# Kernel tuning notes

Measured on AMD Instinct MI355X. Metric: run time of the kernel, lower is better.

Reference implementation:

```python
import jax, jax.numpy as jnp
import numpy as np


def setup_inputs() -> dict:
    key = jax.random.key(0)
    ks = jax.random.split(key, 5)
    B, D, U = 16384, 512, 512
    return {
        "inputs": jax.random.normal(ks[0], (B, D), dtype=jnp.float32),
        "h_prev": jax.random.normal(ks[1], (B, U), dtype=jnp.float32),
        "update_kernel": jax.random.normal(ks[2], (D + U, U), dtype=jnp.float32) * 0.03,
        "reset_kernel": jax.random.normal(ks[3], (D + U, U), dtype=jnp.float32) * 0.03,
        "hidden_kernel": jax.random.normal(ks[4], (D + U, U), dtype=jnp.float32) * 0.03,
        "update_bias": jnp.zeros((U,), dtype=jnp.float32),
        "reset_bias": jnp.zeros((U,), dtype=jnp.float32),
        "hidden_bias": jnp.zeros((U,), dtype=jnp.float32),
    }


def reference(inputs, h_prev, update_kernel, reset_kernel, hidden_kernel,
              update_bias, reset_bias, hidden_bias):
    # fused_input: [B, D+U]
    fused = jnp.concatenate([inputs, h_prev], axis=-1)
    zg = jax.nn.sigmoid(fused @ update_kernel + update_bias)   # update gate [B,U]
    rg = jax.nn.sigmoid(fused @ reset_kernel + reset_bias)     # reset gate  [B,U]
    h_tilde = jnp.tanh(
        jnp.concatenate([inputs, rg * h_prev], axis=-1) @ hidden_kernel + hidden_bias
    )
    ht = (1.0 - zg) * h_prev + zg * h_tilde
    return ht
```

## Files before the change

### kernel.cpp

```cpp
#include <hip/hip_runtime.h>
#include <hip/hip_bf16.h>
#include <math.h>

typedef __attribute__((ext_vector_type(4))) float f32x4;
typedef __bf16 bf16x8 __attribute__((ext_vector_type(8)));
typedef unsigned short u16;
typedef void __attribute__((address_space(1))) * as1p;
typedef void __attribute__((address_space(3))) * as3p;

__device__ __forceinline__ unsigned short f2bf(float f) {
    union { float f; unsigned int u; } v; v.f = f;
    unsigned int u = v.u;
    u += 0x7fffu + ((u >> 16) & 1u);
    return (unsigned short)(u >> 16);
}

__device__ __forceinline__ float bf2f(unsigned short b) {
    union { unsigned int u; float f; } v;
    v.u = ((unsigned int)b) << 16;
    return v.f;
}

__device__ __forceinline__ float fast_tanh(float v) {
    float vc = fminf(fmaxf(v, -15.f), 15.f);
    float e = __expf(2.f * vc);
    return (e - 1.f) / (e + 1.f);
}

__global__ void cvt_xh(const float* __restrict__ x, const float* __restrict__ h,
                       u16* __restrict__ xb, u16* __restrict__ hb, int n4) {
    int i = blockIdx.x * blockDim.x + threadIdx.x;
    int stride = gridDim.x * blockDim.x;
    const float4* x4 = (const float4*)x;
    const float4* h4 = (const float4*)h;
    ushort4* xb4 = (ushort4*)xb;
    ushort4* hb4 = (ushort4*)hb;
    for (; i < n4; i += stride) {
        float4 v = x4[i];
        xb4[i] = make_ushort4(f2bf(v.x), f2bf(v.y), f2bf(v.z), f2bf(v.w));
        float4 w = h4[i];
        hb4[i] = make_ushort4(f2bf(w.x), f2bf(w.y), f2bf(w.z), f2bf(w.w));
    }
}

__global__ void tr_cvt3(const float* __restrict__ s0, const float* __restrict__ s1,
                        const float* __restrict__ s2, u16* __restrict__ d0,
                        u16* __restrict__ d1, u16* __restrict__ d2) {
    __shared__ float t[32][33];
    const float* src = (blockIdx.z == 0) ? s0 : (blockIdx.z == 1) ? s1 : s2;
    u16* dst = (blockIdx.z == 0) ? d0 : (blockIdx.z == 1) ? d1 : d2;
    int n0 = blockIdx.x * 32;
    int k0 = blockIdx.y * 32;
    int tx = threadIdx.x, ty = threadIdx.y;
#pragma unroll
    for (int i = 0; i < 4; ++i)
        t[ty + i * 8][tx] = src[(size_t)(k0 + ty + i * 8) * 512 + n0 + tx];
    __syncthreads();
#pragma unroll
    for (int i = 0; i < 4; ++i)
        dst[(size_t)(n0 + ty + i * 8) * 1024 + k0 + tx] = f2bf(t[tx][ty + i * 8]);
}

__device__ __forceinline__ void stage_sw(const u16* g, int gstride, u16* lds, int tid) {
#pragma unroll
    for (int i = 0; i < 4; ++i) {
        int ob = i * 4096 + ((tid >> 6) << 10);
        int o = ob + ((tid & 63) << 4);
        int row = o >> 7;
        int cb = (o & 127) ^ ((row & 7) << 4);
        const u16* gp = g + (size_t)row * gstride + (cb >> 1);
        __builtin_amdgcn_global_load_lds((as1p)(void*)gp, (as3p)(void*)(lds + (ob >> 1)), 16, 0, 0);
    }
}

__device__ __forceinline__ bf16x8 ld_frag(const u16* region, int r, int kb) {
    int byte = (r << 7) + (kb ^ ((r & 7) << 4));
    return *(const bf16x8*)((const char*)region + byte);
}

__device__ __forceinline__ void compute_tile(const u16* LA, const u16* LB,
                                             int wr, int wc, int l, f32x4 (&acc)[4][4]) {
    int fr = l & 15;
    int kbb = (l >> 4) << 4;
#pragma unroll
    for (int q = 0; q < 2; ++q) {
        bf16x8 a[4], b[4];
#pragma unroll
        for (int m = 0; m < 4; ++m)
            a[m] = ld_frag(LA, wr * 64 + m * 16 + fr, q * 64 + kbb);
#pragma unroll
        for (int n = 0; n < 4; ++n)
            b[n] = ld_frag(LB, wc * 64 + n * 16 + fr, q * 64 + kbb);
#pragma unroll
        for (int m = 0; m < 4; ++m)
#pragma unroll
            for (int n = 0; n < 4; ++n)
                acc[m][n] = __builtin_amdgcn_mfma_f32_16x16x32_bf16(a[m], b[n], acc[m][n], 0, 0, 0);
    }
}

template<typename AF, typename BF>
__device__ __forceinline__ void kloop(AF ga, BF gb, u16* lds, int tid,
                                      int wr, int wc, int l, f32x4 (&acc)[4][4]) {
    stage_sw(ga(0), 512, lds, tid);
    stage_sw(gb(0), 1024, lds + 8192, tid);
    __syncthreads();
#pragma unroll
    for (int i = 0; i < 15; ++i) {
        u16* nxt = lds + ((i + 1) & 1) * 16384;
        const u16* cur = lds + (i & 1) * 16384;
        stage_sw(ga(i + 1), 512, nxt, tid);
        stage_sw(gb(i + 1), 1024, nxt + 8192, tid);
        compute_tile(cur, cur + 8192, wr, wc, l, acc);
        __syncthreads();
    }
    compute_tile(lds + 16384, lds + 16384 + 8192, wr, wc, l, acc);
}

__global__ __launch_bounds__(256) void gemm1_k(
    const u16* __restrict__ Xb, const u16* __restrict__ Hb, const u16* __restrict__ Wt,
    const float* __restrict__ ub, const float* __restrict__ rb_,
    u16* __restrict__ zgb, u16* __restrict__ rgh) {
    __shared__ u16 lds[2 * 16384];
    int tid = threadIdx.x;
    int l = tid & 63, w = tid >> 6;
    int wr = w >> 1, wc = w & 1;
    int bidl = blockIdx.x;
    int swz = (bidl & 7) * 128 + (bidl >> 3);
    int mb = swz >> 3, nb = swz & 7;
    int m0 = mb * 128;
    int n0 = nb * 128;
    f32x4 acc[4][4];
#pragma unroll
    for (int m = 0; m < 4; ++m)
#pragma unroll
        for (int n = 0; n < 4; ++n) acc[m][n] = (f32x4){0.f, 0.f, 0.f, 0.f};

    auto ga = [&](int t) -> const u16* {
        return (t < 8) ? (Xb + (size_t)m0 * 512 + t * 64)
                       : (Hb + (size_t)m0 * 512 + (t - 8) * 64);
    };
    auto gb = [&](int t) -> const u16* {
        return Wt + (size_t)n0 * 1024 + t * 64;
    };
    kloop(ga, gb, lds, tid, wr, wc, l, acc);

    int colb = n0 + wc * 64;
    int rowb = m0 + wr * 64 + ((l >> 4) << 2);
    bool isZ = n0 < 512;
#pragma unroll
    for (int n = 0; n < 4; ++n) {
        int col = colb + n * 16 + (l & 15);
        int c = col & 511;
        float bias = isZ ? ub[c] : rb_[c];
#pragma unroll
        for (int m = 0; m < 4; ++m) {
            int row0 = rowb + m * 16;
#pragma unroll
            for (int r = 0; r < 4; ++r) {
                int row = row0 + r;
                float v = acc[m][n][r] + bias;
                float s = 1.f / (1.f + __expf(-v));
                if (isZ) zgb[(size_t)row * 512 + c] = f2bf(s);
                else     rgh[(size_t)row * 512 + c] = f2bf(s * bf2f(Hb[(size_t)row * 512 + c]));
            }
        }
    }
}

__global__ __launch_bounds__(256) void gemm2_k(
    const u16* __restrict__ Xb, const u16* __restrict__ rgh, const u16* __restrict__ Wt,
    const float* __restrict__ hp, const u16* __restrict__ zgb, const float* __restrict__ hb,
    float* __restrict__ out) {
    __shared__ u16 lds[2 * 16384];
    int tid = threadIdx.x;
    int l = tid & 63, w = tid >> 6;
    int wr = w >> 1, wc = w & 1;
    int bidl = blockIdx.x;
    int swz = (bidl & 7) * 64 + (bidl >> 3);
    int mb = swz >> 2, nb = swz & 3;
    int m0 = mb * 128;
    int n0 = nb * 128;
    f32x4 acc[4][4];
#pragma unroll
    for (int m = 0; m < 4; ++m)
#pragma unroll
        for (int n = 0; n < 4; ++n) acc[m][n] = (f32x4){0.f, 0.f, 0.f, 0.f};

    auto ga = [&](int t) -> const u16* {
        return (t < 8) ? (Xb + (size_t)m0 * 512 + t * 64)
                       : (rgh + (size_t)m0 * 512 + (t - 8) * 64);
    };
    auto gb = [&](int t) -> const u16* {
        return Wt + (size_t)n0 * 1024 + t * 64;
    };
    kloop(ga, gb, lds, tid, wr, wc, l, acc);

    int colb = n0 + wc * 64;
    int rowb = m0 + wr * 64 + ((l >> 4) << 2);
#pragma unroll
    for (int n = 0; n < 4; ++n) {
        int col = colb + n * 16 + (l & 15);
        float bias = hb[col];
#pragma unroll
        for (int m = 0; m < 4; ++m) {
            int row0 = rowb + m * 16;
#pragma unroll
            for (int r = 0; r < 4; ++r) {
                int row = row0 + r;
                float v = acc[m][n][r] + bias;
                float t = fast_tanh(v);
                float h0 = hp[(size_t)row * 512 + col];
                float z = bf2f(zgb[(size_t)row * 512 + col]);
                out[(size_t)row * 512 + col] = h0 + z * (t - h0);
            }
        }
    }
}

extern "C" void kernel_launch(void* const* d_in, const int* in_sizes, int n_in,
                              void* d_out, int out_size, void* d_ws, size_t ws_size,
                              hipStream_t stream) {
    const float* x  = (const float*)d_in[0];
    const float* h  = (const float*)d_in[1];
    const float* wz = (const float*)d_in[2];
    const float* wr = (const float*)d_in[3];
    const float* wh = (const float*)d_in[4];
    const float* ub = (const float*)d_in[5];
    const float* rb = (const float*)d_in[6];
    const float* hb = (const float*)d_in[7];
    float* out = (float*)d_out;

    const int B = 16384;
    char* ws = (char*)d_ws;
    size_t off = 0;
    u16* Xb  = (u16*)(ws + off); off += (size_t)B * 512 * 2;
    u16* Hb  = (u16*)(ws + off); off += (size_t)B * 512 * 2;
    u16* Wzr = (u16*)(ws + off); off += (size_t)1024 * 1024 * 2;
    u16* Wht = (u16*)(ws + off); off += (size_t)512 * 1024 * 2;
    u16* rgh = (u16*)(ws + off); off += (size_t)B * 512 * 2;
    u16* zgb = (u16*)(ws + off); off += (size_t)B * 512 * 2;

    cvt_xh<<<2048, 256, 0, stream>>>(x, h, Xb, Hb, B * 512 / 4);

    dim3 tb(32, 8), tg(16, 32, 3);
    tr_cvt3<<<tg, tb, 0, stream>>>(wz, wr, wh, Wzr, Wzr + (size_t)512 * 1024, Wht);

    gemm1_k<<<1024, 256, 0, stream>>>(Xb, Hb, Wzr, ub, rb, zgb, rgh);
    gemm2_k<<<512, 256, 0, stream>>>(Xb, rgh, Wht, h, zgb, hb, out);
}
```

Before: 119.3 us.

## Stage GEMM epilogues through LDS for vectorized stores and split gate kernels

Each GEMM epilogue now writes its accumulators to LDS and rereads them row-major, so bias, activation and global loads and stores run as 8-wide vectors. The aim is to replace the scattered 2- and 4-byte global accesses of the old epilogue with coalesced ones. The fused z/r GEMM is also split into two separate 512-block kernels, which removes the per-element isZ branch. The cost is an extra kernel launch, extra LDS traffic with two barriers, and likely LDS bank conflicts in the scatter step.

```diff
diff --git a/kernel.cpp b/kernel.cpp
--- a/kernel.cpp
+++ b/kernel.cpp
@@ -3,8 +3,10 @@
 #include <math.h>
 
 typedef __attribute__((ext_vector_type(4))) float f32x4;
+typedef __attribute__((ext_vector_type(8))) float f32x8;
 typedef __bf16 bf16x8 __attribute__((ext_vector_type(8)));
 typedef unsigned short u16;
+typedef u16 u16x8 __attribute__((ext_vector_type(8)));
 typedef void __attribute__((address_space(1))) * as1p;
 typedef void __attribute__((address_space(3))) * as3p;
 
@@ -117,19 +119,33 @@
     compute_tile(lds + 16384, lds + 16384 + 8192, wr, wc, l, acc);
 }
 
-__global__ __launch_bounds__(256) void gemm1_k(
+__device__ __forceinline__ void scatter_acc(float* tf, const f32x4 (&acc)[4][4],
+                                            int wr, int wc, int l) {
+    int colb = wc * 64;
+    int rowb = wr * 64 + ((l >> 4) << 2);
+#pragma unroll
+    for (int n = 0; n < 4; ++n) {
+        int col = colb + n * 16 + (l & 15);
+#pragma unroll
+        for (int m = 0; m < 4; ++m) {
+            int row0 = rowb + m * 16;
+#pragma unroll
+            for (int r = 0; r < 4; ++r)
+                tf[(row0 + r) * 128 + col] = acc[m][n][r];
+        }
+    }
+}
+
+__global__ __launch_bounds__(256) void gz_k(
     const u16* __restrict__ Xb, const u16* __restrict__ Hb, const u16* __restrict__ Wt,
-    const float* __restrict__ ub, const float* __restrict__ rb_,
-    u16* __restrict__ zgb, u16* __restrict__ rgh) {
+    const float* __restrict__ ub, u16* __restrict__ zgb) {
     __shared__ u16 lds[2 * 16384];
     int tid = threadIdx.x;
     int l = tid & 63, w = tid >> 6;
     int wr = w >> 1, wc = w & 1;
-    int bidl = blockIdx.x;
-    int swz = (bidl & 7) * 128 + (bidl >> 3);
-    int mb = swz >> 3, nb = swz & 7;
-    int m0 = mb * 128;
-    int n0 = nb * 128;
+    int swz = (blockIdx.x & 7) * 64 + (blockIdx.x >> 3);
+    int mb = swz >> 2, nb = swz & 3;
+    int m0 = mb * 128, n0 = nb * 128;
     f32x4 acc[4][4];
 #pragma unroll
     for (int m = 0; m < 4; ++m)
@@ -140,35 +156,78 @@
         return (t < 8) ? (Xb + (size_t)m0 * 512 + t * 64)
                        : (Hb + (size_t)m0 * 512 + (t - 8) * 64);
     };
-    auto gb = [&](int t) -> const u16* {
-        return Wt + (size_t)n0 * 1024 + t * 64;
+    auto gb = [&](int t) -> const u16* { return Wt + (size_t)n0 * 1024 + t * 64; };
+    kloop(ga, gb, lds, tid, wr, wc, l, acc);
+
+    __syncthreads();
+    float* tf = (float*)lds;
+    scatter_acc(tf, acc, wr, wc, l);
+    __syncthreads();
+#pragma unroll
+    for (int i = 0; i < 8; ++i) {
+        int chunk = i * 256 + tid;
+        int row = chunk >> 4;
+        int c8 = (chunk & 15) << 3;
+        const float* src = &tf[row * 128 + c8];
+        int gcol = n0 + c8;
+        u16x8 o;
+#pragma unroll
+        for (int j = 0; j < 8; ++j) {
+            float v = src[j] + ub[gcol + j];
+            o[j] = f2bf(1.f / (1.f + __expf(-v)));
+        }
+        *(u16x8*)&zgb[(size_t)(m0 + row) * 512 + gcol] = o;
+    }
+}
+
+__global__ __launch_bounds__(256) void gr_k(
+    const u16* __restrict__ Xb, const u16* __restrict__ Hb, const u16* __restrict__ Wt,
+    const float* __restrict__ rb_, u16* __restrict__ rgh) {
+    __shared__ u16 lds[2 * 16384];
+    int tid = threadIdx.x;
+    int l = tid & 63, w = tid >> 6;
+    int wr = w >> 1, wc = w & 1;
+    int swz = (blockIdx.x & 7) * 64 + (blockIdx.x >> 3);
+    int mb = swz >> 2, nb = swz & 3;
+    int m0 = mb * 128, n0 = nb * 128;
+    f32x4 acc[4][4];
+#pragma unroll
+    for (int m = 0; m < 4; ++m)
+#pragma unroll
+        for (int n = 0; n < 4; ++n) acc[m][n] = (f32x4){0.f, 0.f, 0.f, 0.f};
+
+    auto ga = [&](int t) -> const u16* {
+        return (t < 8) ? (Xb + (size_t)m0 * 512 + t * 64)
+                       : (Hb + (size_t)m0 * 512 + (t - 8) * 64);
     };
+    auto gb = [&](int t) -> const u16* { return Wt + (size_t)n0 * 1024 + t * 64; };
     kloop(ga, gb, lds, tid, wr, wc, l, acc);
 
-    int colb = n0 + wc * 64;
-    int rowb = m0 + wr * 64 + ((l >> 4) << 2);
-    bool isZ = n0 < 512;
-#pragma unroll
-    for (int n = 0; n < 4; ++n) {
-        int col = colb + n * 16 + (l & 15);
-        int c = col & 511;
-        float bias = isZ ? ub[c] : rb_[c];
-#pragma unroll
-        for (int m = 0; m < 4; ++m) {
-            int row0 = rowb + m * 16;
-#pragma unroll
-            for (int r = 0; r < 4; ++r) {
-                int row = row0 + r;
-                float v = acc[m][n][r] + bias;
-                float s = 1.f / (1.f + __expf(-v));
-                if (isZ) zgb[(size_t)row * 512 + c] = f2bf(s);
-                else     rgh[(size_t)row * 512 + c] = f2bf(s * bf2f(Hb[(size_t)row * 512 + c]));
-            }
+    __syncthreads();
+    float* tf = (float*)lds;
+    scatter_acc(tf, acc, wr, wc, l);
+    __syncthreads();
+#pragma unroll
+    for (int i = 0; i < 8; ++i) {
+        int chunk = i * 256 + tid;
+        int row = chunk >> 4;
+        int c8 = (chunk & 15) << 3;
+        const float* src = &tf[row * 128 + c8];
+        int gcol = n0 + c8;
+        size_t gbase = (size_t)(m0 + row) * 512 + gcol;
+        u16x8 h8 = *(const u16x8*)&Hb[gbase];
+        u16x8 o;
+#pragma unroll
+        for (int j = 0; j < 8; ++j) {
+            float v = src[j] + rb_[gcol + j];
+            float s = 1.f / (1.f + __expf(-v));
+            o[j] = f2bf(s * bf2f(h8[j]));
         }
-    }
-}
-
-__global__ __launch_bounds__(256) void gemm2_k(
+        *(u16x8*)&rgh[gbase] = o;
+    }
+}
+
+__global__ __launch_bounds__(256) void gh_k(
     const u16* __restrict__ Xb, const u16* __restrict__ rgh, const u16* __restrict__ Wt,
     const float* __restrict__ hp, const u16* __restrict__ zgb, const float* __restrict__ hb,
     float* __restrict__ out) {
@@ -176,11 +235,9 @@
     int tid = threadIdx.x;
     int l = tid & 63, w = tid >> 6;
     int wr = w >> 1, wc = w & 1;
-    int bidl = blockIdx.x;
-    int swz = (bidl & 7) * 64 + (bidl >> 3);
+    int swz = (blockIdx.x & 7) * 64 + (blockIdx.x >> 3);
     int mb = swz >> 2, nb = swz & 3;
-    int m0 = mb * 128;
-    int n0 = nb * 128;
+    int m0 = mb * 128, n0 = nb * 128;
     f32x4 acc[4][4];
 #pragma unroll
     for (int m = 0; m < 4; ++m)
@@ -191,30 +248,32 @@
         return (t < 8) ? (Xb + (size_t)m0 * 512 + t * 64)
                        : (rgh + (size_t)m0 * 512 + (t - 8) * 64);
     };
-    auto gb = [&](int t) -> const u16* {
-        return Wt + (size_t)n0 * 1024 + t * 64;
-    };
+    auto gb = [&](int t) -> const u16* { return Wt + (size_t)n0 * 1024 + t * 64; };
     kloop(ga, gb, lds, tid, wr, wc, l, acc);
 
-    int colb = n0 + wc * 64;
-    int rowb = m0 + wr * 64 + ((l >> 4) << 2);
-#pragma unroll
-    for (int n = 0; n < 4; ++n) {
-        int col = colb + n * 16 + (l & 15);
-        float bias = hb[col];
-#pragma unroll
-        for (int m = 0; m < 4; ++m) {
-            int row0 = rowb + m * 16;
-#pragma unroll
-            for (int r = 0; r < 4; ++r) {
-                int row = row0 + r;
-                float v = acc[m][n][r] + bias;
-                float t = fast_tanh(v);
-                float h0 = hp[(size_t)row * 512 + col];
-                float z = bf2f(zgb[(size_t)row * 512 + col]);
-                out[(size_t)row * 512 + col] = h0 + z * (t - h0);
-            }
+    __syncthreads();
+    float* tf = (float*)lds;
+    scatter_acc(tf, acc, wr, wc, l);
+    __syncthreads();
+#pragma unroll
+    for (int i = 0; i < 8; ++i) {
+        int chunk = i * 256 + tid;
+        int row = chunk >> 4;
+        int c8 = (chunk & 15) << 3;
+        const float* src = &tf[row * 128 + c8];
+        int gcol = n0 + c8;
+        size_t gbase = (size_t)(m0 + row) * 512 + gcol;
+        f32x8 h8 = *(const f32x8*)&hp[gbase];
+        u16x8 z8 = *(const u16x8*)&zgb[gbase];
+        f32x8 o;
+#pragma unroll
+        for (int j = 0; j < 8; ++j) {
+            float v = src[j] + hb[gcol + j];
+            float t = fast_tanh(v);
+            float z = bf2f(z8[j]);
+            o[j] = h8[j] + z * (t - h8[j]);
         }
+        *(f32x8*)&out[gbase] = o;
     }
 }
 
@@ -236,7 +295,8 @@
     size_t off = 0;
     u16* Xb  = (u16*)(ws + off); off += (size_t)B * 512 * 2;
     u16* Hb  = (u16*)(ws + off); off += (size_t)B * 512 * 2;
-    u16* Wzr = (u16*)(ws + off); off += (size_t)1024 * 1024 * 2;
+    u16* Wzt = (u16*)(ws + off); off += (size_t)512 * 1024 * 2;
+    u16* Wrt = (u16*)(ws + off); off += (size_t)512 * 1024 * 2;
     u16* Wht = (u16*)(ws + off); off += (size_t)512 * 1024 * 2;
     u16* rgh = (u16*)(ws + off); off += (size_t)B * 512 * 2;
     u16* zgb = (u16*)(ws + off); off += (size_t)B * 512 * 2;
@@ -244,8 +304,9 @@
     cvt_xh<<<2048, 256, 0, stream>>>(x, h, Xb, Hb, B * 512 / 4);
 
     dim3 tb(32, 8), tg(16, 32, 3);
-    tr_cvt3<<<tg, tb, 0, stream>>>(wz, wr, wh, Wzr, Wzr + (size_t)512 * 1024, Wht);
-
-    gemm1_k<<<1024, 256, 0, stream>>>(Xb, Hb, Wzr, ub, rb, zgb, rgh);
-    gemm2_k<<<512, 256, 0, stream>>>(Xb, rgh, Wht, h, zgb, hb, out);
-}
+    tr_cvt3<<<tg, tb, 0, stream>>>(wz, wr, wh, Wzt, Wrt, Wht);
+
+    gz_k<<<512, 256, 0, stream>>>(Xb, Hb, Wzt, ub, zgb);
+    gr_k<<<512, 256, 0, stream>>>(Xb, Hb, Wrt, rb, rgh);
+    gh_k<<<512, 256, 0, stream>>>(Xb, rgh, Wht, h, zgb, hb, out);
+}
```

New measurement: 101.7 us. -14.8%, faster.
